# Optimization experiments

Measured on AMD Instinct MI355X. Metric: run time of the kernel, lower is better.

Reference implementation:

```python
import jax, jax.numpy as jnp
import numpy as np

N_NODES = 100000


def gcn_conv(x, src, dst, W, b):
    # PyG GCNConv: linear transform first, then symmetric-normalized aggregation.
    h = x @ W  # [N, out]
    ones = jnp.ones(dst.shape[0], dtype=x.dtype)
    deg = jax.ops.segment_sum(ones, dst, num_segments=N_NODES)  # in-degree incl. self-loops
    dinv = jnp.where(deg > 0, jax.lax.rsqrt(deg), 0.0)
    norm = dinv[src] * dinv[dst]  # [E]
    msg = h[src] * norm[:, None]  # gather + scale
    out = jax.ops.segment_sum(msg, dst, num_segments=N_NODES)  # scatter-add
    return out + b


def add_self_loops(edge_index):
    loops = jnp.arange(N_NODES, dtype=edge_index.dtype)
    src = jnp.concatenate([edge_index[0], loops])
    dst = jnp.concatenate([edge_index[1], loops])
    return src, dst


def setup_inputs() -> dict:
    key = jax.random.key(0)
    k1, k2, k3, k4 = jax.random.split(key, 4)
    N, F, H, C, E = N_NODES, 512, 16, 40, 3200000
    x = jax.random.normal(k1, (N, F), dtype=jnp.float32)
    edge_index = jax.random.randint(k2, (2, E), 0, N, dtype=jnp.int64)
    W1 = jax.random.normal(k3, (F, H), dtype=jnp.float32) * (1.0 / np.sqrt(F))
    b1 = jnp.zeros((H,), dtype=jnp.float32)
    W2 = jax.random.normal(k4, (H, C), dtype=jnp.float32) * (1.0 / np.sqrt(H))
    b2 = jnp.zeros((C,), dtype=jnp.float32)
    return {"x": x, "edge_index": edge_index, "W1": W1, "b1": b1, "W2": W2, "b2": b2}


def reference(x, edge_index, W1, b1, W2, b2):
    src, dst = add_self_loops(edge_index)
    h = gcn_conv(x, src, dst, W1, b1)
    h = jax.nn.relu(h)
    logits = gcn_conv(h, src, dst, W2, b2)
    return jax.nn.log_softmax(logits, axis=1), logits
```

## Files before the change

kernel.cpp:

```cpp
#include <hip/hip_runtime.h>
#include <hip/hip_bf16.h>
#include <math.h>

#define N_NODES 100000
#define F_IN 512
#define H_DIM 16
#define C_DIM 40

#define BSHIFT 9
#define BNODES 512
#define NBUCK 196
#define CHUNK 8192
#define SRC_MASK 0x1FFFF


__global__ void __launch_bounds__(256) bhist_kernel(const int* __restrict__ dst,
                                                    int* __restrict__ BC, int E) {
    __shared__ int cnt[NBUCK];
    int start = blockIdx.x * CHUNK;
    int end = start + CHUNK < E ? start + CHUNK : E;
    for (int i = threadIdx.x; i < NBUCK; i += 256) cnt[i] = 0;
    __syncthreads();
    for (int i = start + threadIdx.x; i < end; i += 256)
        atomicAdd(&cnt[dst[i] >> BSHIFT], 1);
    __syncthreads();
    for (int i = threadIdx.x; i < NBUCK; i += 256) {
        int c = cnt[i];
        if (c) atomicAdd(&BC[i], c);
    }
}


__global__ void __launch_bounds__(256) bscan_kernel(const int* __restrict__ BC,
                                                    int* __restrict__ BO,
                                                    int* __restrict__ cursor,
                                                    int* __restrict__ R, int E, int N) {
    __shared__ int buf[2][256];
    int tid = threadIdx.x;
    int v = (tid < NBUCK) ? BC[tid] : 0;
    int cur = 0;
    buf[0][tid] = v;
    __syncthreads();
    for (int off = 1; off < 256; off <<= 1) {
        int t = buf[cur][tid] + ((tid >= off) ? buf[cur][tid - off] : 0);
        cur ^= 1;
        buf[cur][tid] = t;
        __syncthreads();
    }
    int excl = buf[cur][tid] - v;
    if (tid <= NBUCK) {
        BO[tid] = excl;
        if (tid < NBUCK) cursor[tid] = excl;
    }
    if (tid == 0) R[N] = E;
}


__global__ void __launch_bounds__(256) partition_kernel(const int* __restrict__ src,
                                                        const int* __restrict__ dst,
                                                        int* __restrict__ cursor,
                                                        int* __restrict__ packed, int E) {
    __shared__ int cnt[NBUCK];
    __shared__ int base[NBUCK];
    int start = blockIdx.x * CHUNK;
    int end = start + CHUNK < E ? start + CHUNK : E;
    for (int i = threadIdx.x; i < NBUCK; i += 256) cnt[i] = 0;
    __syncthreads();
    for (int i = start + threadIdx.x; i < end; i += 256)
        atomicAdd(&cnt[dst[i] >> BSHIFT], 1);
    __syncthreads();
    for (int i = threadIdx.x; i < NBUCK; i += 256) {
        int c = cnt[i];
        base[i] = c ? atomicAdd(&cursor[i], c) : 0;
        cnt[i] = 0;
    }
    __syncthreads();
    for (int i = start + threadIdx.x; i < end; i += 256) {
        int d = dst[i];
        int b = d >> BSHIFT;
        int p = base[b] + atomicAdd(&cnt[b], 1);
        packed[p] = ((d & (BNODES - 1)) << 17) | src[i];
    }
}


__global__ void __launch_bounds__(512) sort2_kernel(const int* __restrict__ BO,
                                                    const int* __restrict__ packed,
                                                    int* __restrict__ R,
                                                    float* __restrict__ dinv,
                                                    int* __restrict__ eidx, int N) {
    __shared__ int cnt[BNODES];
    __shared__ int buf[2][BNODES];
    int b = blockIdx.x;
    int tid = threadIdx.x;
    int lo = BO[b], hi = BO[b + 1];
    cnt[tid] = 0;
    __syncthreads();
    for (int e = lo + tid; e < hi; e += 512)
        atomicAdd(&cnt[packed[e] >> 17], 1);
    __syncthreads();
    int deg = cnt[tid];
    int cur = 0;
    buf[0][tid] = deg;
    __syncthreads();
    for (int off = 1; off < 512; off <<= 1) {
        int t = buf[cur][tid] + ((tid >= off) ? buf[cur][tid - off] : 0);
        cur ^= 1;
        buf[cur][tid] = t;
        __syncthreads();
    }
    int excl = lo + buf[cur][tid] - deg;
    int n = (b << BSHIFT) + tid;
    if (n < N) {
        R[n] = excl;
        dinv[n] = rsqrtf((float)(deg + 1));
    }
    cnt[tid] = excl;
    __syncthreads();
    for (int e = lo + tid; e < hi; e += 512) {
        int p = packed[e];
        int pos = atomicAdd(&cnt[p >> 17], 1);
        eidx[pos] = p & SRC_MASK;
    }
}


__global__ void __launch_bounds__(256) gemm1_kernel(const float* __restrict__ x,
                                                    const float* __restrict__ W1,
                                                    const float* __restrict__ dinv,
                                                    float* __restrict__ g1, int N) {
    __shared__ float w[F_IN * H_DIM];
    __shared__ float xs[256 * 33];
    {
        float4* w4s = (float4*)w;
        const float4* W4 = (const float4*)W1;
        for (int i = threadIdx.x; i < F_IN * H_DIM / 4; i += 256) w4s[i] = W4[i];
    }
    int rowbase = blockIdx.x * 256;
    int row = rowbase + threadIdx.x;
    float acc[H_DIM];
#pragma unroll
    for (int k = 0; k < H_DIM; k++) acc[k] = 0.0f;

    int r0 = threadIdx.x >> 3;
    int seg = threadIdx.x & 7;

    for (int kc = 0; kc < F_IN / 32; ++kc) {
        __syncthreads();
#pragma unroll
        for (int rep = 0; rep < 8; ++rep) {
            int r = r0 + rep * 32;
            int gr = rowbase + r;
            float4 v = make_float4(0.f, 0.f, 0.f, 0.f);
            if (gr < N) v = *(const float4*)(x + (size_t)gr * F_IN + kc * 32 + seg * 4);
            float* dp = &xs[r * 33 + seg * 4];
            dp[0] = v.x; dp[1] = v.y; dp[2] = v.z; dp[3] = v.w;
        }
        __syncthreads();
        const float* xr = &xs[threadIdx.x * 33];
        const float* wk = &w[kc * 32 * H_DIM];
#pragma unroll
        for (int j = 0; j < 32; ++j) {
            float s = xr[j];
            const float4* wj = (const float4*)&wk[j * H_DIM];
#pragma unroll
            for (int p = 0; p < 4; p++) {
                float4 wv = wj[p];
                acc[4 * p + 0] += s * wv.x;
                acc[4 * p + 1] += s * wv.y;
                acc[4 * p + 2] += s * wv.z;
                acc[4 * p + 3] += s * wv.w;
            }
        }
    }
    if (row < N) {
        float di = dinv[row];
        float4* o = (float4*)(g1 + (size_t)row * H_DIM);
#pragma unroll
        for (int p = 0; p < 4; p++)
            o[p] = make_float4(acc[4 * p] * di, acc[4 * p + 1] * di,
                               acc[4 * p + 2] * di, acc[4 * p + 3] * di);
    }
}


__global__ void __launch_bounds__(256) agg1_kernel(const int* __restrict__ R,
                                                   const int* __restrict__ eidx,
                                                   const float* __restrict__ g1,
                                                   const float* __restrict__ dinv,
                                                   const float* __restrict__ b1,
                                                   float* __restrict__ g2, int N) {
    int t = blockIdx.x * 256 + threadIdx.x;
    int n = t >> 4;
    if (n >= N) return;
    int k = t & 15;
    int lo = R[n], hi = R[n + 1];
    float sum = g1[t];
    int e = lo;
    for (; e + 8 <= hi; e += 8) {
        int s[8];
        float v[8];
#pragma unroll
        for (int u = 0; u < 8; u++) s[u] = eidx[e + u];
#pragma unroll
        for (int u = 0; u < 8; u++) v[u] = g1[s[u] * H_DIM + k];
#pragma unroll
        for (int u = 0; u < 8; u++) sum += v[u];
    }
    for (; e < hi; ++e) sum += g1[eidx[e] * H_DIM + k];
    float di = dinv[n];
    g2[t] = di * fmaxf(di * sum + b1[k], 0.0f);
}

__global__ void __launch_bounds__(256) agg2_kernel(const int* __restrict__ R,
                                                   const int* __restrict__ eidx,
                                                   const float* __restrict__ g2,
                                                   float* __restrict__ s2, int N) {
    int t = blockIdx.x * 256 + threadIdx.x;
    int n = t >> 4;
    if (n >= N) return;
    int k = t & 15;
    int lo = R[n], hi = R[n + 1];
    float sum = g2[t];
    int e = lo;
    for (; e + 8 <= hi; e += 8) {
        int s[8];
        float v[8];
#pragma unroll
        for (int u = 0; u < 8; u++) s[u] = eidx[e + u];
#pragma unroll
        for (int u = 0; u < 8; u++) v[u] = g2[s[u] * H_DIM + k];
#pragma unroll
        for (int u = 0; u < 8; u++) sum += v[u];
    }
    for (; e < hi; ++e) sum += g2[eidx[e] * H_DIM + k];
    s2[t] = sum;
}


__global__ void __launch_bounds__(256) final_kernel(const float* __restrict__ s2,
                                                    const float* __restrict__ dinv,
                                                    const float* __restrict__ W2,
                                                    const float* __restrict__ b2,
                                                    float* __restrict__ out, int N) {
    __shared__ float w2s[H_DIM * C_DIM];
    __shared__ float b2s[C_DIM];
    __shared__ float stage[256 * 41];
    for (int i = threadIdx.x; i < H_DIM * C_DIM; i += 256) w2s[i] = W2[i];
    if (threadIdx.x < C_DIM) b2s[threadIdx.x] = b2[threadIdx.x];
    __syncthreads();
    int n = blockIdx.x * 256 + threadIdx.x;
    int cn = n < N ? n : 0;
    float di = dinv[cn];
    float v[H_DIM];
    const float4* sv = (const float4*)(s2 + (size_t)cn * H_DIM);
#pragma unroll
    for (int p = 0; p < 4; p++) {
        float4 t = sv[p];
        v[4 * p] = di * t.x; v[4 * p + 1] = di * t.y;
        v[4 * p + 2] = di * t.z; v[4 * p + 3] = di * t.w;
    }
    float lg[C_DIM];
    float m = -1e30f;
    for (int c = 0; c < C_DIM; c++) {
        float a = b2s[c];
#pragma unroll
        for (int k = 0; k < H_DIM; k++) a += v[k] * w2s[k * C_DIM + c];
        lg[c] = a;
        m = fmaxf(m, a);
    }
    float ssum = 0.0f;
    for (int c = 0; c < C_DIM; c++) ssum += __expf(lg[c] - m);
    float lse = m + __logf(ssum);

    size_t base = (size_t)blockIdx.x * 256 * C_DIM;
    size_t lim = (size_t)N * C_DIM;
    for (int c = 0; c < C_DIM; c++) stage[threadIdx.x * 41 + c] = lg[c] - lse;
    __syncthreads();
    for (int i = threadIdx.x; i < 256 * C_DIM; i += 256) {
        int nn = i / C_DIM, c = i - nn * C_DIM;
        size_t g = base + i;
        if (g < lim) out[g] = stage[nn * 41 + c];
    }
    __syncthreads();
    for (int c = 0; c < C_DIM; c++) stage[threadIdx.x * 41 + c] = lg[c];
    __syncthreads();
    for (int i = threadIdx.x; i < 256 * C_DIM; i += 256) {
        int nn = i / C_DIM, c = i - nn * C_DIM;
        size_t g = base + i;
        if (g < lim) out[lim + g] = stage[nn * 41 + c];
    }
}


extern "C" void kernel_launch(void* const* d_in, const int* in_sizes, int n_in,
                              void* d_out, int out_size, void* d_ws, size_t ws_size,
                              hipStream_t stream) {
    const float* x  = (const float*)d_in[0];
    const int* ei   = (const int*)d_in[1];
    const float* W1 = (const float*)d_in[2];
    const float* b1 = (const float*)d_in[3];
    const float* W2 = (const float*)d_in[4];
    const float* b2 = (const float*)d_in[5];
    float* out = (float*)d_out;

    const int N = N_NODES;
    const int E = in_sizes[1] / 2;
    const int* src = ei;
    const int* dst = ei + E;

    int* R      = (int*)d_ws;
    int* BC     = R + 100016;
    int* BO     = BC + 512;
    int* cursor = BO + 256;
    float* dinv = (float*)(cursor + 256);
    int* eidx   = (int*)(dinv + 100016);
    int* packed = eidx + E;
    float* g1   = (float*)packed;
    float* g2   = g1 + 16 * N;
    float* s2   = g1;

    const int NB = (N + 255) / 256;
    const int NCH = (E + CHUNK - 1) / CHUNK;

    hipMemsetAsync(BC, 0, NBUCK * sizeof(int), stream);
    bhist_kernel<<<NCH, 256, 0, stream>>>(dst, BC, E);
    bscan_kernel<<<1, 256, 0, stream>>>(BC, BO, cursor, R, E, N);
    partition_kernel<<<NCH, 256, 0, stream>>>(src, dst, cursor, packed, E);
    sort2_kernel<<<NBUCK, 512, 0, stream>>>(BO, packed, R, dinv, eidx, N);

    gemm1_kernel<<<NB, 256, 0, stream>>>(x, W1, dinv, g1, N);
    agg1_kernel<<<(N * 16 + 255) / 256, 256, 0, stream>>>(R, eidx, g1, dinv, b1, g2, N);
    agg2_kernel<<<(N * 16 + 255) / 256, 256, 0, stream>>>(R, eidx, g2, s2, N);
    final_kernel<<<NB, 256, 0, stream>>>(s2, dinv, W2, b2, out, N);
}
```

Measured before the change: 557.9 us.

## Double-buffer x tiles in GEMM1 and read W1 from global instead of LDS

Restructures the first GEMM kernel to prefetch the next 16-column slab of x into registers while computing on the current LDS buffer, using two LDS buffers and one barrier per step. It drops the 32 KB LDS copy of W1 and reads weights directly from global memory as uniform float4 loads, which cuts LDS use and may raise occupancy. The risk is more iterations with smaller k-chunks and weight reads going through the cache instead of LDS.

```diff
diff --git a/kernel.cpp b/kernel.cpp
--- a/kernel.cpp
+++ b/kernel.cpp
@@ -129,50 +129,64 @@
                                                     const float* __restrict__ W1,
                                                     const float* __restrict__ dinv,
                                                     float* __restrict__ g1, int N) {
-    __shared__ float w[F_IN * H_DIM];
-    __shared__ float xs[256 * 33];
-    {
-        float4* w4s = (float4*)w;
-        const float4* W4 = (const float4*)W1;
-        for (int i = threadIdx.x; i < F_IN * H_DIM / 4; i += 256) w4s[i] = W4[i];
-    }
+    __shared__ float xs[2][256 * 17];
+    int tid = threadIdx.x;
     int rowbase = blockIdx.x * 256;
-    int row = rowbase + threadIdx.x;
+    int r0 = tid >> 2;
+    int seg = tid & 3;
+    float4 pv[4];
+
+#pragma unroll
+    for (int rep = 0; rep < 4; ++rep) {
+        int gr = rowbase + r0 + rep * 64;
+        pv[rep] = make_float4(0.f, 0.f, 0.f, 0.f);
+        if (gr < N) pv[rep] = *(const float4*)(x + (size_t)gr * F_IN + seg * 4);
+    }
+#pragma unroll
+    for (int rep = 0; rep < 4; ++rep) {
+        float* dp = &xs[0][(r0 + rep * 64) * 17 + seg * 4];
+        dp[0] = pv[rep].x; dp[1] = pv[rep].y; dp[2] = pv[rep].z; dp[3] = pv[rep].w;
+    }
+
     float acc[H_DIM];
 #pragma unroll
     for (int k = 0; k < H_DIM; k++) acc[k] = 0.0f;
 
-    int r0 = threadIdx.x >> 3;
-    int seg = threadIdx.x & 7;
-
-    for (int kc = 0; kc < F_IN / 32; ++kc) {
-        __syncthreads();
-#pragma unroll
-        for (int rep = 0; rep < 8; ++rep) {
-            int r = r0 + rep * 32;
-            int gr = rowbase + r;
-            float4 v = make_float4(0.f, 0.f, 0.f, 0.f);
-            if (gr < N) v = *(const float4*)(x + (size_t)gr * F_IN + kc * 32 + seg * 4);
-            float* dp = &xs[r * 33 + seg * 4];
-            dp[0] = v.x; dp[1] = v.y; dp[2] = v.z; dp[3] = v.w;
+    for (int kc = 0; kc < F_IN / 16; ++kc) {
+        if (kc + 1 < F_IN / 16) {
+#pragma unroll
+            for (int rep = 0; rep < 4; ++rep) {
+                int gr = rowbase + r0 + rep * 64;
+                pv[rep] = make_float4(0.f, 0.f, 0.f, 0.f);
+                if (gr < N)
+                    pv[rep] = *(const float4*)(x + (size_t)gr * F_IN + (kc + 1) * 16 + seg * 4);
+            }
         }
         __syncthreads();
-        const float* xr = &xs[threadIdx.x * 33];
-        const float* wk = &w[kc * 32 * H_DIM];
-#pragma unroll
-        for (int j = 0; j < 32; ++j) {
+        const float* xr = &xs[kc & 1][tid * 17];
+        const float4* Wk = (const float4*)(W1 + kc * 16 * H_DIM);
+#pragma unroll
+        for (int j = 0; j < 16; ++j) {
             float s = xr[j];
-            const float4* wj = (const float4*)&wk[j * H_DIM];
-#pragma unroll
-            for (int p = 0; p < 4; p++) {
-                float4 wv = wj[p];
+#pragma unroll
+            for (int p = 0; p < 4; ++p) {
+                float4 wv = Wk[j * 4 + p];
                 acc[4 * p + 0] += s * wv.x;
                 acc[4 * p + 1] += s * wv.y;
                 acc[4 * p + 2] += s * wv.z;
                 acc[4 * p + 3] += s * wv.w;
             }
         }
-    }
+        if (kc + 1 < F_IN / 16) {
+#pragma unroll
+            for (int rep = 0; rep < 4; ++rep) {
+                float* dp = &xs[(kc + 1) & 1][(r0 + rep * 64) * 17 + seg * 4];
+                dp[0] = pv[rep].x; dp[1] = pv[rep].y; dp[2] = pv[rep].z; dp[3] = pv[rep].w;
+            }
+        }
+    }
+
+    int row = rowbase + tid;
     if (row < N) {
         float di = dinv[row];
         float4* o = (float4*)(g1 + (size_t)row * H_DIM);
```

Result: faster. 542.9 us (-2.7%).
